# Optimization experiments

Measured on AMD Instinct MI355X. Metric: run time of the kernel, lower is better.

## Reference

```python
import jax, jax.numpy as jnp
import numpy as np

B, LS, LH, D1, D2 = 16, 1024, 1024, 1024, 1024


def setup_inputs() -> dict:
    key = jax.random.key(0)
    k1, k2, k3 = jax.random.split(key, 3)
    S = jax.random.normal(k1, (B, LS, D1), dtype=jnp.float32)
    H = jax.random.normal(k2, (B, LH, D2), dtype=jnp.float32)
    pad_mask = jnp.zeros((B, LS, LH), dtype=jnp.float32)  # additive mask
    W_w = jax.random.normal(k3, (D2, D1), dtype=jnp.float32) / np.sqrt(D1)
    W_b = jnp.zeros((D2,), dtype=jnp.float32)
    return {"S": S, "H": H, "pad_mask": pad_mask, "W_w": W_w, "W_b": W_b}


def reference(S, H, pad_mask, W_w, W_b):
    # Linear projection: S_ = S @ W^T + b  -> [B, LS, D2]
    S_ = jnp.einsum('bsd,ed->bse', S, W_w) + W_b
    # Unscaled dot-product scores: [B, LS, LH]
    score = jnp.einsum('bse,bte->bst', S_, H)
    score = score + pad_mask  # additive pad mask
    score = jax.nn.softmax(score, axis=-1)
    # Weighted sum of H: [B, LS, D2]
    out = jnp.einsum('bst,bte->bse', score, H)
    return out
```

## Files before the change

kernel.cpp:

```cpp
#include <hip/hip_runtime.h>
#include <stdint.h>

typedef _Float16 half8 __attribute__((ext_vector_type(8)));
typedef float floatx4 __attribute__((ext_vector_type(4)));

__device__ __forceinline__ uint16_t f16bits(_Float16 h) {
  union { _Float16 f; uint16_t u; } x; x.f = h; return x.u;
}

__device__ __forceinline__ void g2l16(const void* g, void* l) {
  __builtin_amdgcn_global_load_lds((const __attribute__((address_space(1))) void*)g,
                                   (__attribute__((address_space(3))) void*)l,
                                   16, 0, 0);
}

__global__ __launch_bounds__(256) void split_f16_kernel(
    const float* __restrict__ x, uint16_t* __restrict__ hi,
    uint16_t* __restrict__ lo, int n4) {
  int i = blockIdx.x * 256 + threadIdx.x;
  if (i >= n4) return;
  float4 v = ((const float4*)x)[i];
  ushort4 h, l;
  _Float16 a;
  a = (_Float16)v.x; h.x = f16bits(a); l.x = f16bits((_Float16)(v.x - (float)a));
  a = (_Float16)v.y; h.y = f16bits(a); l.y = f16bits((_Float16)(v.y - (float)a));
  a = (_Float16)v.z; h.z = f16bits(a); l.z = f16bits((_Float16)(v.z - (float)a));
  a = (_Float16)v.w; h.w = f16bits(a); l.w = f16bits((_Float16)(v.w - (float)a));
  ((ushort4*)hi)[i] = h;
  ((ushort4*)lo)[i] = l;
}

template <bool SPLIT, int MODE>
__global__ __launch_bounds__(256, 4) void gemm_bt(
    const uint16_t* __restrict__ Ahi, const uint16_t* __restrict__ Alo,
    const uint16_t* __restrict__ Bhi, const uint16_t* __restrict__ Blo,
    uint16_t* __restrict__ Chi, uint16_t* __restrict__ Clo,
    float* __restrict__ Cf, const float* __restrict__ mask,
    const float* __restrict__ bias, int N, int K,
    long batchA, long batchB, long batchC) {
  constexpr int NBUF = SPLIT ? 2 : 1;
  constexpr int LOI = SPLIT ? 1 : 0;
  __shared__ __align__(16) uint16_t sA[NBUF][128 * 32];
  __shared__ __align__(16) uint16_t sB[NBUF][128 * 32];

  const int tid = threadIdx.x;
  const int lane = tid & 63;
  const int w = tid >> 6;
  const int wr = w >> 1, wc = w & 1;
  const int quad = lane >> 4, l16 = lane & 15;

  const int m0 = blockIdx.y * 128;
  const int n0 = blockIdx.x * 128;
  const size_t zA = (size_t)blockIdx.z * batchA;
  const size_t zB = (size_t)blockIdx.z * batchB;
  const size_t zC = (size_t)blockIdx.z * batchC;

  const int r0 = w * 32 + (lane >> 2);
  const int ldc = (((lane & 3) ^ ((lane >> 2) & 3)) * 16);

  const char* gAh0 = (const char*)(Ahi + zA + (size_t)(m0 + r0) * K) + ldc;
  const char* gAh1 = gAh0 + (size_t)16 * K * 2;
  const char* gBh0 = (const char*)(Bhi + zB + (size_t)(n0 + r0) * K) + ldc;
  const char* gBh1 = gBh0 + (size_t)16 * K * 2;
  const char* gAl0 = gAh0; const char* gAl1 = gAh1;
  const char* gBl0 = gBh0; const char* gBl1 = gBh1;
  if constexpr (SPLIT) {
    gAl0 = (const char*)(Alo + zA + (size_t)(m0 + r0) * K) + ldc;
    gAl1 = gAl0 + (size_t)16 * K * 2;
    gBl0 = (const char*)(Blo + zB + (size_t)(n0 + r0) * K) + ldc;
    gBl1 = gBl0 + (size_t)16 * K * 2;
  }
  uint16_t* lA0 = &sA[0][(w * 32) * 32];
  uint16_t* lA1 = &sA[0][(w * 32 + 16) * 32];
  uint16_t* lB0 = &sB[0][(w * 32) * 32];
  uint16_t* lB1 = &sB[0][(w * 32 + 16) * 32];
  uint16_t* lA0l = &sA[LOI][(w * 32) * 32];
  uint16_t* lA1l = &sA[LOI][(w * 32 + 16) * 32];
  uint16_t* lB0l = &sB[LOI][(w * 32) * 32];
  uint16_t* lB1l = &sB[LOI][(w * 32 + 16) * 32];

  const int aoff = (wr * 64 + l16) * 32 + ((quad ^ (l16 & 3)) * 8);
  const int boff = (wc * 64 + l16) * 32 + ((quad ^ (l16 & 3)) * 8);

  floatx4 acc[4][4];
  floatx4 zero = {0.f, 0.f, 0.f, 0.f};
#pragma unroll
  for (int i = 0; i < 4; ++i)
#pragma unroll
    for (int j = 0; j < 4; ++j) acc[i][j] = zero;

  const int nkt = K >> 5;
  for (int kt = 0; kt < nkt; ++kt) {
    const int kb = kt * 64;
    g2l16(gAh0 + kb, lA0);
    g2l16(gAh1 + kb, lA1);
    g2l16(gBh0 + kb, lB0);
    g2l16(gBh1 + kb, lB1);
    if constexpr (SPLIT) {
      g2l16(gAl0 + kb, lA0l);
      g2l16(gAl1 + kb, lA1l);
      g2l16(gBl0 + kb, lB0l);
      g2l16(gBl1 + kb, lB1l);
    }
    __syncthreads();

    half8 fa[4];
#pragma unroll
    for (int i = 0; i < 4; ++i) fa[i] = *(const half8*)&sA[0][aoff + i * 512];
    if constexpr (SPLIT) {
      half8 fbl[4];
#pragma unroll
      for (int j = 0; j < 4; ++j) fbl[j] = *(const half8*)&sB[1][boff + j * 512];
#pragma unroll
      for (int i = 0; i < 4; ++i)
#pragma unroll
        for (int j = 0; j < 4; ++j)
          acc[i][j] = __builtin_amdgcn_mfma_f32_16x16x32_f16(fa[i], fbl[j], acc[i][j], 0, 0, 0);
    }
    half8 fbh[4];
#pragma unroll
    for (int j = 0; j < 4; ++j) fbh[j] = *(const half8*)&sB[0][boff + j * 512];
#pragma unroll
    for (int i = 0; i < 4; ++i)
#pragma unroll
      for (int j = 0; j < 4; ++j)
        acc[i][j] = __builtin_amdgcn_mfma_f32_16x16x32_f16(fa[i], fbh[j], acc[i][j], 0, 0, 0);
    if constexpr (SPLIT) {
      half8 fal[4];
#pragma unroll
      for (int i = 0; i < 4; ++i) fal[i] = *(const half8*)&sA[1][aoff + i * 512];
#pragma unroll
      for (int i = 0; i < 4; ++i)
#pragma unroll
        for (int j = 0; j < 4; ++j)
          acc[i][j] = __builtin_amdgcn_mfma_f32_16x16x32_f16(fal[i], fbh[j], acc[i][j], 0, 0, 0);
    }
    __syncthreads();
  }

  const int crow0 = m0 + wr * 64 + quad * 4;
  const int ccol0 = n0 + wc * 64 + l16;
#pragma unroll
  for (int j = 0; j < 4; ++j) {
    const int col = ccol0 + j * 16;
    float bj = 0.f;
    if constexpr (MODE == 0) bj = bias[col];
#pragma unroll
    for (int i = 0; i < 4; ++i) {
#pragma unroll
      for (int r = 0; r < 4; ++r) {
        const int row = crow0 + i * 16 + r;
        const size_t idx = zC + (size_t)row * N + col;
        float v = acc[i][j][r];
        if constexpr (MODE == 0) {
          v += bj;
          _Float16 h = (_Float16)v;
          Chi[idx] = f16bits(h);
          Clo[idx] = f16bits((_Float16)(v - (float)h));
        } else if constexpr (MODE == 1) {
          Cf[idx] = v + mask[idx];
        } else {
          Cf[idx] = v;
        }
      }
    }
  }
}

__global__ __launch_bounds__(256) void softmax_kernel(
    const float* __restrict__ sc, uint16_t* __restrict__ p) {
  const int row = blockIdx.x;
  const float* x = sc + (size_t)row * 1024;
  const int t = threadIdx.x;
  float4 v = ((const float4*)x)[t];
  float m = fmaxf(fmaxf(v.x, v.y), fmaxf(v.z, v.w));
#pragma unroll
  for (int off = 32; off; off >>= 1) m = fmaxf(m, __shfl_xor(m, off));
  __shared__ float redm[4];
  __shared__ float reds[4];
  const int wv = t >> 6, ln = t & 63;
  if (ln == 0) redm[wv] = m;
  __syncthreads();
  m = fmaxf(fmaxf(redm[0], redm[1]), fmaxf(redm[2], redm[3]));
  float e0 = __expf(v.x - m), e1 = __expf(v.y - m);
  float e2 = __expf(v.z - m), e3 = __expf(v.w - m);
  float s = e0 + e1 + e2 + e3;
#pragma unroll
  for (int off = 32; off; off >>= 1) s += __shfl_xor(s, off);
  if (ln == 0) reds[wv] = s;
  __syncthreads();
  s = reds[0] + reds[1] + reds[2] + reds[3];
  float inv = 1.f / s;
  ushort4 o;
  o.x = f16bits((_Float16)(e0 * inv));
  o.y = f16bits((_Float16)(e1 * inv));
  o.z = f16bits((_Float16)(e2 * inv));
  o.w = f16bits((_Float16)(e3 * inv));
  ((ushort4*)(p + (size_t)row * 1024))[t] = o;
}

__global__ __launch_bounds__(256) void transpose_f16_kernel(
    const float* __restrict__ src, uint16_t* __restrict__ dst) {
  __shared__ uint16_t tile[64][65];
  const int e0 = blockIdx.x * 64;
  const int t0 = blockIdx.y * 64;
  const size_t bb = (size_t)blockIdx.z << 20;
  const int r = threadIdx.x >> 4;
  const int c = (threadIdx.x & 15) * 4;
#pragma unroll
  for (int it = 0; it < 4; ++it) {
    const int tr = r + it * 16;
    float4 v = *(const float4*)(src + bb + (size_t)(t0 + tr) * 1024 + e0 + c);
    tile[c + 0][tr] = f16bits((_Float16)v.x);
    tile[c + 1][tr] = f16bits((_Float16)v.y);
    tile[c + 2][tr] = f16bits((_Float16)v.z);
    tile[c + 3][tr] = f16bits((_Float16)v.w);
  }
  __syncthreads();
#pragma unroll
  for (int it = 0; it < 4; ++it) {
    const int er = r + it * 16;
    ushort4 o;
    o.x = tile[er][c + 0];
    o.y = tile[er][c + 1];
    o.z = tile[er][c + 2];
    o.w = tile[er][c + 3];
    *(ushort4*)(dst + bb + (size_t)(e0 + er) * 1024 + t0 + c) = o;
  }
}

extern "C" void kernel_launch(void* const* d_in, const int* in_sizes, int n_in,
                              void* d_out, int out_size, void* d_ws, size_t ws_size,
                              hipStream_t stream) {
  (void)in_sizes; (void)n_in; (void)out_size; (void)ws_size;
  const float* S    = (const float*)d_in[0];
  const float* H    = (const float*)d_in[1];
  const float* mask = (const float*)d_in[2];
  const float* Ww   = (const float*)d_in[3];
  const float* Wb   = (const float*)d_in[4];
  float* out = (float*)d_out;
  char* ws = (char*)d_ws;
  const size_t MB = 1024ull * 1024ull;

  uint16_t* Whi  = (uint16_t*)(ws + 0 * MB);
  uint16_t* Wlo  = (uint16_t*)(ws + 2 * MB);
  uint16_t* Pjhi = (uint16_t*)(ws + 4 * MB);
  uint16_t* Pjlo = (uint16_t*)(ws + 36 * MB);
  uint16_t* Hhi  = (uint16_t*)(ws + 68 * MB);
  uint16_t* Hlo  = (uint16_t*)(ws + 100 * MB);
  uint16_t* Shi  = (uint16_t*)(ws + 132 * MB);
  uint16_t* Slo  = (uint16_t*)(ws + 164 * MB);
  float*    SC   = (float*)(ws + 132 * MB);
  uint16_t* PR   = (uint16_t*)(ws + 68 * MB);
  uint16_t* HT   = (uint16_t*)(ws + 100 * MB);

  split_f16_kernel<<<16384, 256, 0, stream>>>(S, Shi, Slo, 4 * 1024 * 1024);
  split_f16_kernel<<<16384, 256, 0, stream>>>(H, Hhi, Hlo, 4 * 1024 * 1024);
  split_f16_kernel<<<1024, 256, 0, stream>>>(Ww, Whi, Wlo, 256 * 1024);

  gemm_bt<true, 0><<<dim3(8, 128, 1), 256, 0, stream>>>(
      Shi, Slo, Whi, Wlo, Pjhi, Pjlo, nullptr, nullptr, Wb,
      1024, 1024, 0, 0, 0);
  gemm_bt<true, 1><<<dim3(8, 8, 16), 256, 0, stream>>>(
      Pjhi, Pjlo, Hhi, Hlo, nullptr, nullptr, SC, mask, nullptr,
      1024, 1024, 1048576, 1048576, 1048576);
  softmax_kernel<<<16384, 256, 0, stream>>>(SC, PR);
  transpose_f16_kernel<<<dim3(16, 16, 16), 256, 0, stream>>>(H, HT);
  gemm_bt<false, 2><<<dim3(8, 8, 16), 256, 0, stream>>>(
      PR, nullptr, HT, nullptr, nullptr, nullptr, out, nullptr, nullptr,
      1024, 1024, 1048576, 1048576, 1048576);
}
```

Measured before the change: 582.2 us.

## Load split-GEMM low halves directly from global and swizzle block order

```diff
diff --git a/kernel.cpp b/kernel.cpp
--- a/kernel.cpp
+++ b/kernel.cpp
@@ -38,10 +38,8 @@
     float* __restrict__ Cf, const float* __restrict__ mask,
     const float* __restrict__ bias, int N, int K,
     long batchA, long batchB, long batchC) {
-  constexpr int NBUF = SPLIT ? 2 : 1;
-  constexpr int LOI = SPLIT ? 1 : 0;
-  __shared__ __align__(16) uint16_t sA[NBUF][128 * 32];
-  __shared__ __align__(16) uint16_t sB[NBUF][128 * 32];
+  __shared__ __align__(16) uint16_t sA[128 * 32];
+  __shared__ __align__(16) uint16_t sB[128 * 32];
 
   const int tid = threadIdx.x;
   const int lane = tid & 63;
@@ -49,8 +47,12 @@
   const int wr = w >> 1, wc = w & 1;
   const int quad = lane >> 4, l16 = lane & 15;
 
-  const int m0 = blockIdx.y * 128;
-  const int n0 = blockIdx.x * 128;
+  const int lin = blockIdx.y * 8 + blockIdx.x;
+  const int bx = (lin >> 3) & 7;
+  const int by = (lin & 7) | ((lin >> 6) << 3);
+
+  const int m0 = by * 128;
+  const int n0 = bx * 128;
   const size_t zA = (size_t)blockIdx.z * batchA;
   const size_t zB = (size_t)blockIdx.z * batchB;
   const size_t zC = (size_t)blockIdx.z * batchC;
@@ -62,22 +64,18 @@
   const char* gAh1 = gAh0 + (size_t)16 * K * 2;
   const char* gBh0 = (const char*)(Bhi + zB + (size_t)(n0 + r0) * K) + ldc;
   const char* gBh1 = gBh0 + (size_t)16 * K * 2;
-  const char* gAl0 = gAh0; const char* gAl1 = gAh1;
-  const char* gBl0 = gBh0; const char* gBl1 = gBh1;
+  uint16_t* lA0 = &sA[(w * 32) * 32];
+  uint16_t* lA1 = &sA[(w * 32 + 16) * 32];
+  uint16_t* lB0 = &sB[(w * 32) * 32];
+  uint16_t* lB1 = &sB[(w * 32 + 16) * 32];
+
+  const char* pAlo = nullptr;
+  const char* pBlo = nullptr;
   if constexpr (SPLIT) {
-    gAl0 = (const char*)(Alo + zA + (size_t)(m0 + r0) * K) + ldc;
-    gAl1 = gAl0 + (size_t)16 * K * 2;
-    gBl0 = (const char*)(Blo + zB + (size_t)(n0 + r0) * K) + ldc;
-    gBl1 = gBl0 + (size_t)16 * K * 2;
-  }
-  uint16_t* lA0 = &sA[0][(w * 32) * 32];
-  uint16_t* lA1 = &sA[0][(w * 32 + 16) * 32];
-  uint16_t* lB0 = &sB[0][(w * 32) * 32];
-  uint16_t* lB1 = &sB[0][(w * 32 + 16) * 32];
-  uint16_t* lA0l = &sA[LOI][(w * 32) * 32];
-  uint16_t* lA1l = &sA[LOI][(w * 32 + 16) * 32];
-  uint16_t* lB0l = &sB[LOI][(w * 32) * 32];
-  uint16_t* lB1l = &sB[LOI][(w * 32 + 16) * 32];
+    pAlo = (const char*)(Alo + zA + (size_t)(m0 + wr * 64 + l16) * K) + quad * 16;
+    pBlo = (const char*)(Blo + zB + (size_t)(n0 + wc * 64 + l16) * K) + quad * 16;
+  }
+  const size_t fstride = (size_t)32 * K;
 
   const int aoff = (wr * 64 + l16) * 32 + ((quad ^ (l16 & 3)) * 8);
   const int boff = (wc * 64 + l16) * 32 + ((quad ^ (l16 & 3)) * 8);
@@ -96,39 +94,34 @@
     g2l16(gAh1 + kb, lA1);
     g2l16(gBh0 + kb, lB0);
     g2l16(gBh1 + kb, lB1);
-    if constexpr (SPLIT) {
-      g2l16(gAl0 + kb, lA0l);
-      g2l16(gAl1 + kb, lA1l);
-      g2l16(gBl0 + kb, lB0l);
-      g2l16(gBl1 + kb, lB1l);
-    }
     __syncthreads();
 
-    half8 fa[4];
-#pragma unroll
-    for (int i = 0; i < 4; ++i) fa[i] = *(const half8*)&sA[0][aoff + i * 512];
+    half8 fa[4], fbh[4];
+#pragma unroll
+    for (int i = 0; i < 4; ++i) fa[i] = *(const half8*)&sA[aoff + i * 512];
+#pragma unroll
+    for (int j = 0; j < 4; ++j) fbh[j] = *(const half8*)&sB[boff + j * 512];
+
+#pragma unroll
+    for (int i = 0; i < 4; ++i)
+#pragma unroll
+      for (int j = 0; j < 4; ++j)
+        acc[i][j] = __builtin_amdgcn_mfma_f32_16x16x32_f16(fa[i], fbh[j], acc[i][j], 0, 0, 0);
+
     if constexpr (SPLIT) {
       half8 fbl[4];
 #pragma unroll
-      for (int j = 0; j < 4; ++j) fbl[j] = *(const half8*)&sB[1][boff + j * 512];
+      for (int j = 0; j < 4; ++j)
+        fbl[j] = *(const half8*)(pBlo + (size_t)j * fstride + kb);
 #pragma unroll
       for (int i = 0; i < 4; ++i)
 #pragma unroll
         for (int j = 0; j < 4; ++j)
           acc[i][j] = __builtin_amdgcn_mfma_f32_16x16x32_f16(fa[i], fbl[j], acc[i][j], 0, 0, 0);
-    }
-    half8 fbh[4];
-#pragma unroll
-    for (int j = 0; j < 4; ++j) fbh[j] = *(const half8*)&sB[0][boff + j * 512];
-#pragma unroll
-    for (int i = 0; i < 4; ++i)
-#pragma unroll
-      for (int j = 0; j < 4; ++j)
-        acc[i][j] = __builtin_amdgcn_mfma_f32_16x16x32_f16(fa[i], fbh[j], acc[i][j], 0, 0, 0);
-    if constexpr (SPLIT) {
       half8 fal[4];
 #pragma unroll
-      for (int i = 0; i < 4; ++i) fal[i] = *(const half8*)&sA[1][aoff + i * 512];
+      for (int i = 0; i < 4; ++i)
+        fal[i] = *(const half8*)(pAlo + (size_t)i * fstride + kb);
 #pragma unroll
       for (int i = 0; i < 4; ++i)
 #pragma unroll
```

Result: slower. 663.7 us (+14.0%).

## Fuse H split with transpose and remap GEMM grids for XCD-local batch reuse

Applied to the files above, without the earlier changes.

```diff
diff --git a/kernel.cpp b/kernel.cpp
--- a/kernel.cpp
+++ b/kernel.cpp
@@ -30,7 +30,47 @@
   ((ushort4*)lo)[i] = l;
 }
 
-template <bool SPLIT, int MODE>
+__global__ __launch_bounds__(256) void split_h_kernel(
+    const float* __restrict__ src, uint16_t* __restrict__ hi,
+    uint16_t* __restrict__ lo, uint16_t* __restrict__ ht) {
+  __shared__ uint16_t tile[64][65];
+  const int e0 = blockIdx.x * 64;
+  const int t0 = blockIdx.y * 64;
+  const size_t bb = (size_t)blockIdx.z << 20;
+  const int r = threadIdx.x >> 4;
+  const int c = (threadIdx.x & 15) * 4;
+#pragma unroll
+  for (int it = 0; it < 4; ++it) {
+    const int tr = r + it * 16;
+    const size_t idx = bb + (size_t)(t0 + tr) * 1024 + e0 + c;
+    float4 v = *(const float4*)(src + idx);
+    ushort4 h, l;
+    _Float16 a;
+    a = (_Float16)v.x; h.x = f16bits(a); l.x = f16bits((_Float16)(v.x - (float)a));
+    a = (_Float16)v.y; h.y = f16bits(a); l.y = f16bits((_Float16)(v.y - (float)a));
+    a = (_Float16)v.z; h.z = f16bits(a); l.z = f16bits((_Float16)(v.z - (float)a));
+    a = (_Float16)v.w; h.w = f16bits(a); l.w = f16bits((_Float16)(v.w - (float)a));
+    *(ushort4*)(hi + idx) = h;
+    *(ushort4*)(lo + idx) = l;
+    tile[c + 0][tr] = h.x;
+    tile[c + 1][tr] = h.y;
+    tile[c + 2][tr] = h.z;
+    tile[c + 3][tr] = h.w;
+  }
+  __syncthreads();
+#pragma unroll
+  for (int it = 0; it < 4; ++it) {
+    const int er = r + it * 16;
+    ushort4 o;
+    o.x = tile[er][c + 0];
+    o.y = tile[er][c + 1];
+    o.z = tile[er][c + 2];
+    o.w = tile[er][c + 3];
+    *(ushort4*)(ht + bb + (size_t)(e0 + er) * 1024 + t0 + c) = o;
+  }
+}
+
+template <bool SPLIT, int MODE, int GMAP>
 __global__ __launch_bounds__(256, 4) void gemm_bt(
     const uint16_t* __restrict__ Ahi, const uint16_t* __restrict__ Alo,
     const uint16_t* __restrict__ Bhi, const uint16_t* __restrict__ Blo,
@@ -49,11 +89,17 @@
   const int wr = w >> 1, wc = w & 1;
   const int quad = lane >> 4, l16 = lane & 15;
 
-  const int m0 = blockIdx.y * 128;
-  const int n0 = blockIdx.x * 128;
-  const size_t zA = (size_t)blockIdx.z * batchA;
-  const size_t zB = (size_t)blockIdx.z * batchB;
-  const size_t zC = (size_t)blockIdx.z * batchC;
+  int m_t, n_t, z;
+  if constexpr (GMAP == 0) {
+    m_t = blockIdx.x; n_t = blockIdx.y; z = 0;
+  } else {
+    z = blockIdx.x; m_t = blockIdx.y >> 3; n_t = blockIdx.y & 7;
+  }
+  const int m0 = m_t * 128;
+  const int n0 = n_t * 128;
+  const size_t zA = (size_t)z * batchA;
+  const size_t zB = (size_t)z * batchB;
+  const size_t zC = (size_t)z * batchC;
 
   const int r0 = w * 32 + (lane >> 2);
   const int ldc = (((lane & 3) ^ ((lane >> 2) & 3)) * 16);
@@ -232,7 +278,7 @@
 extern "C" void kernel_launch(void* const* d_in, const int* in_sizes, int n_in,
                               void* d_out, int out_size, void* d_ws, size_t ws_size,
                               hipStream_t stream) {
-  (void)in_sizes; (void)n_in; (void)out_size; (void)ws_size;
+  (void)in_sizes; (void)n_in; (void)out_size;
   const float* S    = (const float*)d_in[0];
   const float* H    = (const float*)d_in[1];
   const float* mask = (const float*)d_in[2];
@@ -252,21 +298,30 @@
   uint16_t* Slo  = (uint16_t*)(ws + 164 * MB);
   float*    SC   = (float*)(ws + 132 * MB);
   uint16_t* PR   = (uint16_t*)(ws + 68 * MB);
-  uint16_t* HT   = (uint16_t*)(ws + 100 * MB);
+
+  const bool roomy = ws_size >= 229ull * MB;
+  uint16_t* HT = roomy ? (uint16_t*)(ws + 196 * MB)
+                       : (uint16_t*)(ws + 100 * MB);
 
   split_f16_kernel<<<16384, 256, 0, stream>>>(S, Shi, Slo, 4 * 1024 * 1024);
-  split_f16_kernel<<<16384, 256, 0, stream>>>(H, Hhi, Hlo, 4 * 1024 * 1024);
   split_f16_kernel<<<1024, 256, 0, stream>>>(Ww, Whi, Wlo, 256 * 1024);
-
-  gemm_bt<true, 0><<<dim3(8, 128, 1), 256, 0, stream>>>(
+  if (roomy) {
+    split_h_kernel<<<dim3(16, 16, 16), 256, 0, stream>>>(H, Hhi, Hlo, HT);
+  } else {
+    split_f16_kernel<<<16384, 256, 0, stream>>>(H, Hhi, Hlo, 4 * 1024 * 1024);
+  }
+
+  gemm_bt<true, 0, 0><<<dim3(128, 8, 1), 256, 0, stream>>>(
       Shi, Slo, Whi, Wlo, Pjhi, Pjlo, nullptr, nullptr, Wb,
       1024, 1024, 0, 0, 0);
-  gemm_bt<true, 1><<<dim3(8, 8, 16), 256, 0, stream>>>(
+  gemm_bt<true, 1, 1><<<dim3(16, 64, 1), 256, 0, stream>>>(
       Pjhi, Pjlo, Hhi, Hlo, nullptr, nullptr, SC, mask, nullptr,
       1024, 1024, 1048576, 1048576, 1048576);
   softmax_kernel<<<16384, 256, 0, stream>>>(SC, PR);
-  transpose_f16_kernel<<<dim3(16, 16, 16), 256, 0, stream>>>(H, HT);
-  gemm_bt<false, 2><<<dim3(8, 8, 16), 256, 0, stream>>>(
+  if (!roomy) {
+    transpose_f16_kernel<<<dim3(16, 16, 16), 256, 0, stream>>>(H, HT);
+  }
+  gemm_bt<false, 2, 1><<<dim3(16, 64, 1), 256, 0, stream>>>(
       PR, nullptr, HT, nullptr, nullptr, nullptr, out, nullptr, nullptr,
       1024, 1024, 1048576, 1048576, 1048576);
 }
```

Measured after the change: 523.0 us. 1.11x faster.
